# Kernel optimization log

Hardware: AMD Instinct MI355X
Metric: run time of the kernel (lower is better)

Reference implementation:

```python
import jax, jax.numpy as jnp
import numpy as np

K = 16          # max_points
S = 3           # num_scales
DM = 256        # d_model
KD = 16         # k_dim geometric projection
TAU = 1e-4
LN_EPS = 1e-5


def _boundaries():
    edges = [(i, j) for i in range(K) for j in range(i + 1, K)]
    tris = [(i, j, k) for i in range(K) for j in range(i + 1, K) for k in range(j + 1, K)]
    E, T = len(edges), len(tris)
    B1 = np.zeros((K, E), np.float32)
    for e, (i, j) in enumerate(edges):
        B1[i, e] = -1.0
        B1[j, e] = 1.0
    eidx = {e: n for n, e in enumerate(edges)}
    B2 = np.zeros((E, T), np.float32)
    for t, (i, j, k) in enumerate(tris):
        B2[eidx[(j, k)], t] = 1.0
        B2[eidx[(i, k)], t] = -1.0
        B2[eidx[(i, j)], t] = 1.0
    ei = np.array([e[0] for e in edges])
    ej = np.array([e[1] for e in edges])
    tij = np.array([eidx[(a, b)] for a, b, c in tris])
    tjk = np.array([eidx[(b, c)] for a, b, c in tris])
    tik = np.array([eidx[(a, c)] for a, b, c in tris])
    return (jnp.asarray(B1), jnp.asarray(B2), jnp.asarray(np.abs(B1)),
            jnp.asarray(ei), jnp.asarray(ej), jnp.asarray(tij), jnp.asarray(tjk), jnp.asarray(tik))

_B1, _B2, _ABS, _EI, _EJ, _TIJ, _TJK, _TIK = _boundaries()
E = _B1.shape[1]  # 120


def _ln(x, g, b):
    m = jnp.mean(x, -1, keepdims=True)
    v = jnp.mean((x - m) ** 2, -1, keepdims=True)
    return (x - m) * jax.lax.rsqrt(v + LN_EPS) * g + b


def setup_inputs() -> dict:
    key = jax.random.key(0)
    ks = jax.random.split(key, 12)
    B = 1024
    p = lambda k, *sh: 0.02 * jax.random.normal(k, sh, dtype=jnp.float32)
    return {
        'x': jax.random.normal(ks[0], (B, K, DM), dtype=jnp.float32),
        'mask': jnp.ones((B, K), dtype=jnp.float32),
        'Wg': p(ks[1], DM, KD), 'bg': jnp.zeros((KD,), jnp.float32),
        'log_scales': jnp.linspace(-1.5, 1.5, S, dtype=jnp.float32),
        'Wv': p(ks[2], DM, DM * S), 'bv': jnp.zeros((DM * S,), jnp.float32),
        'We': p(ks[3], DM, DM * S), 'be': jnp.zeros((DM * S,), jnp.float32),
        'Wo': p(ks[4], DM * S * 2, DM), 'bo': jnp.zeros((DM,), jnp.float32),
        'ln1_g': jnp.ones((DM,), jnp.float32), 'ln1_b': jnp.zeros((DM,), jnp.float32),
        'ln2_g': jnp.ones((DM,), jnp.float32), 'ln2_b': jnp.zeros((DM,), jnp.float32),
        'Wf1': p(ks[5], DM, DM * 4), 'bf1': jnp.zeros((DM * 4,), jnp.float32),
        'Wf2': p(ks[6], DM * 4, DM), 'bf2': jnp.zeros((DM,), jnp.float32),
    }


def reference(x, mask, Wg, bg, log_scales, Wv, bv, We, be, Wo, bo,
              ln1_g, ln1_b, ln2_g, ln2_b, Wf1, bf1, Wf2, bf2):
    B = x.shape[0]
    xn = _ln(x, ln1_g, ln1_b)
    P = xn @ Wg + bg                                   # [B,K,KD]
    m2 = mask[:, :, None] * mask[:, None, :]           # [B,K,K]
    p2 = jnp.sum(P * P, -1)
    Dsq = jnp.maximum(p2[:, :, None] + p2[:, None, :] - 2.0 * jnp.einsum('bkc,blc->bkl', P, P), 0.0) * m2
    sig2 = jnp.exp(log_scales) ** 2                    # [S]
    V0 = (xn @ Wv + bv).reshape(B, K, S, DM).transpose(0, 2, 1, 3)   # [B,S,K,D]
    Eraw = jnp.einsum('ke,bkd->bed', _ABS, xn)         # [B,E,D]
    Ein = (Eraw @ We + be).reshape(B, E, S, DM).transpose(0, 2, 1, 3)  # [B,S,E,D]
    aff = jnp.exp(-Dsq[:, None] / (2.0 * sig2[None, :, None, None] + 1e-8)) * m2[:, None]  # [B,S,K,K]
    W1 = aff[:, :, _EI, _EJ]                           # [B,S,E]
    W2 = W1[:, :, _TIJ] * W1[:, :, _TJK] * W1[:, :, _TIK]  # [B,S,T]
    L0 = jnp.einsum('ke,bse,le->bskl', _B1, W1, _B1) + TAU * jnp.eye(K, dtype=x.dtype)
    node_upd = jnp.einsum('bskl,bsld->bskd', L0, V0)
    term_down = jnp.einsum('ke,bk,kf->bef', _B1, mask, _B1)
    term_up = jnp.einsum('et,bst,ft->bsef', _B2, W2, _B2)
    L1 = term_down[:, None] + term_up + TAU * jnp.eye(E, dtype=x.dtype)
    edge_msg = jnp.einsum('bsef,bsfd->bsed', L1, Ein)
    edge_upd = jnp.einsum('ke,bsed->bskd', _ABS, edge_msg)
    nu = node_upd.transpose(0, 2, 1, 3).reshape(B, K, S * DM)
    eu = edge_upd.transpose(0, 2, 1, 3).reshape(B, K, S * DM)
    x = x + (jnp.concatenate([nu, eu], -1) @ Wo + bo)  # residual + attn_out (dropout=eval noop)
    h = _ln(x, ln2_g, ln2_b)
    return x + (jax.nn.gelu(h @ Wf1 + bf1, approximate=False) @ Wf2 + bf2)
```

## Files before the change

kernel.cpp:

```cpp
#include <hip/hip_runtime.h>
#include <hip/hip_bf16.h>
#include <cstdint>
#include <cstddef>

#define TAU 1e-4f
#define LN_EPS 1e-5f

typedef unsigned short ushort_t;
typedef unsigned int uint_t;
typedef __attribute__((ext_vector_type(8))) short short8;
typedef __attribute__((ext_vector_type(4))) float f32x4;

__device__ __forceinline__ ushort_t f2bf(float f) {
    union { float f; unsigned int u; } c; c.f = f;
    unsigned int r = (c.u + 0x7fffu + ((c.u >> 16) & 1u)) >> 16;
    return (ushort_t)r;
}
__device__ __forceinline__ void glds16(const void* g, void* l) {
    __builtin_amdgcn_global_load_lds((const __attribute__((address_space(1))) unsigned int*)g,
                                     (__attribute__((address_space(3))) unsigned int*)l,
                                     16, 0, 0);
}

__global__ __launch_bounds__(256) void kA(
    const float* __restrict__ xg, const float* __restrict__ maskg,
    const float* __restrict__ Wg, const float* __restrict__ bg,
    const float* __restrict__ ls, const float* __restrict__ g1,
    const float* __restrict__ b1, ushort_t* __restrict__ Mcat,
    float* __restrict__ gbuf,
    const float* __restrict__ Wv, const float* __restrict__ We,
    const float* __restrict__ Wo, const float* __restrict__ bv,
    const float* __restrict__ be, const float* __restrict__ Wf1,
    const float* __restrict__ Wf2, ushort_t* __restrict__ WcatT,
    ushort_t* __restrict__ Wf1T, ushort_t* __restrict__ Wf2T,
    float* __restrict__ cvpart, float* __restrict__ beWo) {
    __shared__ __align__(16) float POOL[7968];
    const int tid = threadIdx.x;

    if (blockIdx.x >= 1024) {
        const int id = blockIdx.x - 1024;
        if (id < 384) {
            float (*rowS)[256] = (float(*)[256])POOL;
            const int q0 = (id & 63) * 4;
            const int w = id >> 6;
            const int half = w / 3, s = w - half * 3;
            const float* src = half ? We : Wv;
#pragma unroll
            for (int r = 0; r < 4; ++r)
                rowS[r][tid] = src[(size_t)(q0 + r) * 768 + s * 256 + tid];
            __syncthreads();
            const float* wo = Wo + (size_t)(half * 768 + s * 256) * 256 + tid;
            float a0 = 0.f, a1 = 0.f, a2 = 0.f, a3 = 0.f;
            for (int d = 0; d < 256; ++d) {
                float wv = wo[(size_t)d * 256];
                a0 += rowS[0][d] * wv; a1 += rowS[1][d] * wv;
                a2 += rowS[2][d] * wv; a3 += rowS[3][d] * wv;
            }
            const int rt = half * 3 + s;
            ushort4 pk;
            pk.x = f2bf(a0); pk.y = f2bf(a1); pk.z = f2bf(a2); pk.w = f2bf(a3);
            *(ushort4*)&WcatT[(size_t)tid * 1536 + rt * 256 + q0] = pk;
        } else if (id < 390) {
            const int w = id - 384;
            const int half = w / 3, s = w - half * 3;
            const float* vec = half ? be : bv;
            POOL[tid] = vec[s * 256 + tid];
            __syncthreads();
            const float* wo = Wo + (size_t)(half * 768 + s * 256) * 256 + tid;
            float acc = 0.f;
            for (int d = 0; d < 256; ++d) acc += POOL[d] * wo[(size_t)d * 256];
            if (half) beWo[s * 256 + tid] = acc;
            else cvpart[s * 256 + tid] = acc;
        } else {
            float (*tS)[65] = (float(*)[65])POOL;
            const float* src; ushort_t* dst;
            int sr0, sc0, ss, dr0, dc0, ds_;
            if (id < 454) {
                int t = id - 390; int ki = t & 3, ni = t >> 2;
                src = Wf1; ss = 1024; sr0 = ki * 64; sc0 = ni * 64;
                dst = Wf1T; ds_ = 256; dr0 = ni * 64; dc0 = ki * 64;
            } else {
                int t = id - 454; int ki = t >> 2, ni = t & 3;
                src = Wf2; ss = 256; sr0 = ki * 64; sc0 = ni * 64;
                dst = Wf2T; ds_ = 1024; dr0 = ni * 64; dc0 = ki * 64;
            }
            const int rl = tid >> 6, cl = tid & 63;
#pragma unroll
            for (int p = 0; p < 16; ++p) {
                int r = p * 4 + rl;
                tS[r][cl] = src[(size_t)(sr0 + r) * ss + sc0 + cl];
            }
            __syncthreads();
#pragma unroll
            for (int p = 0; p < 16; ++p) {
                int r = p * 4 + rl;
                dst[(size_t)(dr0 + r) * ds_ + dc0 + cl] = f2bf(tS[cl][r]);
            }
        }
        return;
    }

    const int b = blockIdx.x;
    float (*XS)[260] = (float(*)[260])POOL;
    float (*WgTh)[132] = (float(*)[132])(POOL + 4160);
    float* Ms = POOL + 4160;
    float (*Wh)[16][17] = (float(*)[16][17])(POOL + 6272);
    float* Ts = POOL + 7088;
    float (*Pl)[17] = (float(*)[17])(POOL + 7136);
    float (*dotm)[17] = (float(*)[17])(POOL + 7408);
    float (*DsqS)[17] = (float(*)[17])(POOL + 7680);
    float* mk = POOL + 7952;

    const float* xb = xg + (size_t)b * 4096;
#pragma unroll
    for (int i = 0; i < 4; ++i) {
        int idx = tid * 4 + i * 1024;
        int k = idx >> 8, c = idx & 255;
        float4 v = *(const float4*)&xb[idx];
        XS[k][c] = v.x; XS[k][c + 1] = v.y; XS[k][c + 2] = v.z; XS[k][c + 3] = v.w;
    }
    if (tid < 16) mk[tid] = maskg[b * 16 + tid];
    __syncthreads();

    {
        const int k = tid >> 4, c = tid & 15;
        float s = 0.f;
#pragma unroll
        for (int j = 0; j < 16; ++j) s += XS[k][c + 16 * j];
        for (int off = 8; off; off >>= 1) s += __shfl_down(s, off, 16);
        float mean = __shfl(s, 0, 16) * (1.f / 256.f);
        float vs = 0.f;
#pragma unroll
        for (int j = 0; j < 16; ++j) { float d = XS[k][c + 16 * j] - mean; vs += d * d; }
        for (int off = 8; off; off >>= 1) vs += __shfl_down(vs, off, 16);
        float rstd = rsqrtf(__shfl(vs, 0, 16) * (1.f / 256.f) + LN_EPS);
#pragma unroll
        for (int j = 0; j < 16; ++j) {
            int cc = c + 16 * j;
            XS[k][cc] = (XS[k][cc] - mean) * rstd * g1[cc] + b1[cc];
        }
    }
    __syncthreads();

    {
        const int k = tid >> 4, c = tid & 15;
        const int ql = tid >> 1, hf = tid & 1;
        float acc = bg[c];
        {
            const float4* wp = (const float4*)(Wg + ql * 16 + hf * 8);
            float4 w0 = wp[0], w1 = wp[1];
            WgTh[hf * 8 + 0][ql] = w0.x; WgTh[hf * 8 + 1][ql] = w0.y;
            WgTh[hf * 8 + 2][ql] = w0.z; WgTh[hf * 8 + 3][ql] = w0.w;
            WgTh[hf * 8 + 4][ql] = w1.x; WgTh[hf * 8 + 5][ql] = w1.y;
            WgTh[hf * 8 + 6][ql] = w1.z; WgTh[hf * 8 + 7][ql] = w1.w;
        }
        __syncthreads();
        const float4* wp2 = (const float4*)(Wg + (128 + ql) * 16 + hf * 8);
        float4 w20 = wp2[0], w21 = wp2[1];
#pragma unroll
        for (int q4 = 0; q4 < 32; ++q4) {
            float4 wv = *(const float4*)&WgTh[c][q4 * 4];
            float4 xv = *(const float4*)&XS[k][q4 * 4];
            acc += wv.x * xv.x + wv.y * xv.y + wv.z * xv.z + wv.w * xv.w;
        }
        __syncthreads();
        WgTh[hf * 8 + 0][ql] = w20.x; WgTh[hf * 8 + 1][ql] = w20.y;
        WgTh[hf * 8 + 2][ql] = w20.z; WgTh[hf * 8 + 3][ql] = w20.w;
        WgTh[hf * 8 + 4][ql] = w21.x; WgTh[hf * 8 + 5][ql] = w21.y;
        WgTh[hf * 8 + 6][ql] = w21.z; WgTh[hf * 8 + 7][ql] = w21.w;
        __syncthreads();
#pragma unroll
        for (int q4 = 0; q4 < 32; ++q4) {
            float4 wv = *(const float4*)&WgTh[c][q4 * 4];
            float4 xv = *(const float4*)&XS[k][128 + q4 * 4];
            acc += wv.x * xv.x + wv.y * xv.y + wv.z * xv.z + wv.w * xv.w;
        }
        Pl[k][c] = acc;
    }
    __syncthreads();
    const int k = tid >> 4, m = tid & 15;
    {
        float d = 0.f;
#pragma unroll
        for (int c = 0; c < 16; ++c) d += Pl[k][c] * Pl[m][c];
        dotm[k][m] = d;
    }
    __syncthreads();
    {
        float v = dotm[k][k] + dotm[m][m] - 2.f * dotm[k][m];
        DsqS[k][m] = fmaxf(v, 0.f) * mk[k] * mk[m];
    }
    {
        float d = DsqS[k][m];
        float mm = mk[k] * mk[m];
#pragma unroll
        for (int s = 0; s < 3; ++s) {
            float i2 = 1.f / (2.f * expf(2.f * ls[s]) + 1e-8f);
            Wh[s][k][m] = (k == m) ? 0.f : expf(-d * i2) * mm;
        }
    }
    __syncthreads();
    if (tid < 48) {
        int s = tid >> 4, j = tid & 15;
        float t = 0.f;
        for (int i = 0; i < j; ++i) {
            float d = 0.f;
            for (int jj = j + 1; jj < 16; ++jj) d += Wh[s][j][jj] * Wh[s][i][jj];
            t += Wh[s][i][j] * d;
        }
        Ts[s * 16 + j] = t;
    }
    __syncthreads();
    float gd = 0.f;
#pragma unroll
    for (int o = 0; o < 16; ++o) {
        if (o == m) continue;
        int u = o < m ? o : m, v = o < m ? m : o;
        float gu = (u == k) ? (float)(2 * k - 15) : ((u > k) ? 1.f : -1.f);
        float gv = (v == k) ? (float)(2 * k - 15) : ((v > k) ? 1.f : -1.f);
        gd += -gu * mk[u] + gv * mk[v];
        if (u == k || v == k) gd += TAU;
    }
#pragma unroll
    for (int s = 0; s < 3; ++s) {
        float rs = 0.f;
#pragma unroll
        for (int o = 0; o < 16; ++o) rs += Wh[s][k][o];
        float l0 = (k == m) ? (rs + TAU) : -Wh[s][k][m];
        float G = gd + ((k == m) ? 4.f * Ts[s * 16 + k] : 0.f);
        Ms[s * 256 + tid] = l0;
        Ms[768 + s * 256 + tid] = G;
        float gg = G;
        for (int off = 8; off; off >>= 1) gg += __shfl_down(gg, off, 16);
        if (m == 0) gbuf[b * 48 + k * 3 + s] = 0.5f * gg;
    }
    __syncthreads();

    {
        const int q2 = (tid & 127) * 2;
        const int rtbase = (tid >> 7) * 3;
        float xv0[16], xv1[16];
#pragma unroll
        for (int l = 0; l < 16; ++l) { xv0[l] = XS[l][q2]; xv1[l] = XS[l][q2 + 1]; }
        const size_t obase = (size_t)b * 16 * 1536;
#pragma unroll
        for (int rtt = 0; rtt < 3; ++rtt) {
            const int rt = rtbase + rtt;
#pragma unroll
            for (int kk = 0; kk < 16; ++kk) {
                const float4* mp = (const float4*)&Ms[rt * 256 + kk * 16];
                float4 m0 = mp[0], m1 = mp[1], m2 = mp[2], m3 = mp[3];
                float a0 = m0.x * xv0[0] + m0.y * xv0[1] + m0.z * xv0[2] + m0.w * xv0[3]
                         + m1.x * xv0[4] + m1.y * xv0[5] + m1.z * xv0[6] + m1.w * xv0[7]
                         + m2.x * xv0[8] + m2.y * xv0[9] + m2.z * xv0[10] + m2.w * xv0[11]
                         + m3.x * xv0[12] + m3.y * xv0[13] + m3.z * xv0[14] + m3.w * xv0[15];
                float a1 = m0.x * xv1[0] + m0.y * xv1[1] + m0.z * xv1[2] + m0.w * xv1[3]
                         + m1.x * xv1[4] + m1.y * xv1[5] + m1.z * xv1[6] + m1.w * xv1[7]
                         + m2.x * xv1[8] + m2.y * xv1[9] + m2.z * xv1[10] + m2.w * xv1[11]
                         + m3.x * xv1[12] + m3.y * xv1[13] + m3.z * xv1[14] + m3.w * xv1[15];
                uint_t pk = (uint_t)f2bf(a0) | ((uint_t)f2bf(a1) << 16);
                *(uint_t*)&Mcat[obase + (size_t)kk * 1536 + rt * 256 + q2] = pk;
            }
        }
    }
}

__device__ __forceinline__ void gemm64_db(
    const ushort_t* __restrict__ A, const ushort_t* __restrict__ Bt,
    int Kdim, int m0, int n0, f32x4 acc[2][4],
    ushort_t (*As0)[32], ushort_t (*As1)[32],
    ushort_t (*Bs0)[32], ushort_t (*Bs1)[32]) {
    const int tid = threadIdx.x;
    const int wave = tid >> 6, lane = tid & 63;
    const int lq = lane >> 4, lr = lane & 15;
    const int wm = wave >> 1, wn = wave & 1;
    const int r = tid >> 2, ca = (tid & 3) << 3;
    const ushort_t* Ag  = A  + (size_t)(m0 + r) * Kdim + ca;
    const ushort_t* Bg0 = Bt + (size_t)(n0 + r) * Kdim + ca;
    const ushort_t* Bg1 = Bt + (size_t)(n0 + 64 + r) * Kdim + ca;
    char* aD0  = (char*)As0 + wave * 1024;
    char* aD1  = (char*)As1 + wave * 1024;
    char* b0D0 = (char*)Bs0 + wave * 1024;
    char* b0D1 = (char*)Bs0 + 4096 + wave * 1024;
    char* b1D0 = (char*)Bs1 + wave * 1024;
    char* b1D1 = (char*)Bs1 + 4096 + wave * 1024;

    glds16(Ag, aD0); glds16(Bg0, b0D0); glds16(Bg1, b0D1);

    for (int kt = 0; kt < Kdim; kt += 64) {
        {
            const int kn = kt + 32;
            if (kn < Kdim) {
                glds16(Ag + kn, aD1); glds16(Bg0 + kn, b1D0); glds16(Bg1 + kn, b1D1);
                asm volatile("s_waitcnt vmcnt(3)" ::: "memory");
            } else {
                asm volatile("s_waitcnt vmcnt(0)" ::: "memory");
            }
            __builtin_amdgcn_s_barrier();
            short8 af[2], bfr[4];
#pragma unroll
            for (int i = 0; i < 2; ++i) af[i] = *(const short8*)&As0[wm * 32 + i * 16 + lr][lq * 8];
#pragma unroll
            for (int j = 0; j < 4; ++j) bfr[j] = *(const short8*)&Bs0[wn * 64 + j * 16 + lr][lq * 8];
#pragma unroll
            for (int i = 0; i < 2; ++i)
#pragma unroll
                for (int j = 0; j < 4; ++j)
                    acc[i][j] = __builtin_amdgcn_mfma_f32_16x16x32_bf16(af[i], bfr[j], acc[i][j], 0, 0, 0);
            asm volatile("s_waitcnt lgkmcnt(0)" ::: "memory");
            __builtin_amdgcn_s_barrier();
        }
        {
            const int kn = kt + 64;
            if (kn < Kdim) {
                glds16(Ag + kn, aD0); glds16(Bg0 + kn, b0D0); glds16(Bg1 + kn, b0D1);
                asm volatile("s_waitcnt vmcnt(3)" ::: "memory");
            } else {
                asm volatile("s_waitcnt vmcnt(0)" ::: "memory");
            }
            __builtin_amdgcn_s_barrier();
            short8 af[2], bfr[4];
#pragma unroll
            for (int i = 0; i < 2; ++i) af[i] = *(const short8*)&As1[wm * 32 + i * 16 + lr][lq * 8];
#pragma unroll
            for (int j = 0; j < 4; ++j) bfr[j] = *(const short8*)&Bs1[wn * 64 + j * 16 + lr][lq * 8];
#pragma unroll
            for (int i = 0; i < 2; ++i)
#pragma unroll
                for (int j = 0; j < 4; ++j)
                    acc[i][j] = __builtin_amdgcn_mfma_f32_16x16x32_bf16(af[i], bfr[j], acc[i][j], 0, 0, 0);
            asm volatile("s_waitcnt lgkmcnt(0)" ::: "memory");
            __builtin_amdgcn_s_barrier();
        }
    }
}

__global__ __launch_bounds__(256) void kZY_gemm(
    const ushort_t* __restrict__ Mcat, const ushort_t* __restrict__ WcatT,
    const float* __restrict__ xin, const float* __restrict__ bo,
    const float* __restrict__ cvpart, const float* __restrict__ beWo,
    const float* __restrict__ gbuf, float* __restrict__ xp) {
    __shared__ ushort_t As0[64][32], As1[64][32];
    __shared__ ushort_t Bs0[128][32], Bs1[128][32];
    __shared__ float cvS[128], bewS[3][128], gblk[64][3];
    const int tid = threadIdx.x;
    const int m0 = blockIdx.x * 64, n0 = blockIdx.y * 128;
    if (tid < 128) {
        int n = n0 + tid;
        cvS[tid] = bo[n] + TAU * (cvpart[n] + cvpart[256 + n] + cvpart[512 + n]);
        bewS[0][tid] = beWo[n];
        bewS[1][tid] = beWo[256 + n];
        bewS[2][tid] = beWo[512 + n];
    }
    if (tid < 192) { int rr = tid / 3, s = tid - rr * 3; gblk[rr][s] = gbuf[(size_t)(m0 + rr) * 3 + s]; }
    f32x4 acc[2][4] = {};
    gemm64_db(Mcat, WcatT, 1536, m0, n0, acc, As0, As1, Bs0, Bs1);
    const int wave = tid >> 6, lane = tid & 63, lq = lane >> 4, lr = lane & 15;
    const int wm = wave >> 1, wn = wave & 1;
#pragma unroll
    for (int i = 0; i < 2; ++i)
#pragma unroll
        for (int j = 0; j < 4; ++j) {
            int nl = wn * 64 + j * 16 + lr;
#pragma unroll
            for (int v = 0; v < 4; ++v) {
                int rl = wm * 32 + i * 16 + lq * 4 + v;
                size_t idx = (size_t)(m0 + rl) * 256 + n0 + nl;
                xp[idx] = acc[i][j][v] + xin[idx] + cvS[nl] +
                          gblk[rl][0] * bewS[0][nl] + gblk[rl][1] * bewS[1][nl] +
                          gblk[rl][2] * bewS[2][nl];
            }
        }
}

__global__ __launch_bounds__(256) void k_ln2(const float* __restrict__ xp,
                                             const float* __restrict__ g2,
                                             const float* __restrict__ b2,
                                             ushort_t* __restrict__ h) {
    const int tid = threadIdx.x;
    const int row = blockIdx.x * 4 + (tid >> 6);
    const int lane = tid & 63;
    const float* xr = xp + (size_t)row * 256;
    float v0 = xr[lane], v1 = xr[lane + 64], v2 = xr[lane + 128], v3 = xr[lane + 192];
    float s = v0 + v1 + v2 + v3;
    for (int m = 32; m; m >>= 1) s += __shfl_xor(s, m, 64);
    float mean = s * (1.f / 256.f);
    float d0 = v0 - mean, d1 = v1 - mean, d2 = v2 - mean, d3 = v3 - mean;
    float q = d0 * d0 + d1 * d1 + d2 * d2 + d3 * d3;
    for (int m = 32; m; m >>= 1) q += __shfl_xor(q, m, 64);
    float rstd = rsqrtf(q * (1.f / 256.f) + LN_EPS);
    ushort_t* hr = h + (size_t)row * 256;
    hr[lane] = f2bf(d0 * rstd * g2[lane] + b2[lane]);
    hr[lane + 64] = f2bf(d1 * rstd * g2[lane + 64] + b2[lane + 64]);
    hr[lane + 128] = f2bf(d2 * rstd * g2[lane + 128] + b2[lane + 128]);
    hr[lane + 192] = f2bf(d3 * rstd * g2[lane + 192] + b2[lane + 192]);
}

__global__ __launch_bounds__(256) void k3_gemm(const ushort_t* __restrict__ h,
                                               const ushort_t* __restrict__ Wf1T,
                                               const float* __restrict__ bf1,
                                               ushort_t* __restrict__ F1g) {
    __shared__ ushort_t As0[64][32], As1[64][32];
    __shared__ ushort_t Bs0[128][32], Bs1[128][32];
    const int tid = threadIdx.x;
    const int m0 = blockIdx.x * 64, n0 = blockIdx.y * 128;
    f32x4 acc[2][4] = {};
    gemm64_db(h, Wf1T, 256, m0, n0, acc, As0, As1, Bs0, Bs1);
    const int wave = tid >> 6, lane = tid & 63, lq = lane >> 4, lr = lane & 15;
    const int wm = wave >> 1, wn = wave & 1;
#pragma unroll
    for (int i = 0; i < 2; ++i)
#pragma unroll
        for (int j = 0; j < 4; ++j) {
            int n = n0 + wn * 64 + j * 16 + lr;
            float bn = bf1[n];
#pragma unroll
            for (int v = 0; v < 4; ++v) {
                int rg = m0 + wm * 32 + i * 16 + lq * 4 + v;
                float u = acc[i][j][v] + bn;
                float gl = 0.5f * u * (1.f + erff(u * 0.70710678118f));
                F1g[(size_t)rg * 1024 + n] = f2bf(gl);
            }
        }
}

__global__ __launch_bounds__(256) void k4_gemm(const ushort_t* __restrict__ F1g,
                                               const ushort_t* __restrict__ Wf2T,
                                               const float* __restrict__ bf2,
                                               const float* __restrict__ xp,
                                               float* __restrict__ out) {
    __shared__ ushort_t As0[64][32], As1[64][32];
    __shared__ ushort_t Bs0[128][32], Bs1[128][32];
    const int tid = threadIdx.x;
    const int m0 = blockIdx.x * 64, n0 = blockIdx.y * 128;
    f32x4 acc[2][4] = {};
    gemm64_db(F1g, Wf2T, 1024, m0, n0, acc, As0, As1, Bs0, Bs1);
    const int wave = tid >> 6, lane = tid & 63, lq = lane >> 4, lr = lane & 15;
    const int wm = wave >> 1, wn = wave & 1;
#pragma unroll
    for (int i = 0; i < 2; ++i)
#pragma unroll
        for (int j = 0; j < 4; ++j) {
            int n = n0 + wn * 64 + j * 16 + lr;
            float bn = bf2[n];
#pragma unroll
            for (int v = 0; v < 4; ++v) {
                size_t idx = (size_t)(m0 + wm * 32 + i * 16 + lq * 4 + v) * 256 + n;
                out[idx] = xp[idx] + acc[i][j][v] + bn;
            }
        }
}

extern "C" void kernel_launch(void* const* d_in, const int* in_sizes, int n_in,
                              void* d_out, int out_size, void* d_ws, size_t ws_size,
                              hipStream_t stream) {
    const float* x = (const float*)d_in[0];
    const float* mask = (const float*)d_in[1];
    const float* Wg = (const float*)d_in[2];
    const float* bg = (const float*)d_in[3];
    const float* ls = (const float*)d_in[4];
    const float* Wv = (const float*)d_in[5];
    const float* bv = (const float*)d_in[6];
    const float* We = (const float*)d_in[7];
    const float* be = (const float*)d_in[8];
    const float* Wo = (const float*)d_in[9];
    const float* bo = (const float*)d_in[10];
    const float* g1 = (const float*)d_in[11];
    const float* b1 = (const float*)d_in[12];
    const float* g2 = (const float*)d_in[13];
    const float* b2 = (const float*)d_in[14];
    const float* Wf1 = (const float*)d_in[15];
    const float* bf1 = (const float*)d_in[16];
    const float* Wf2 = (const float*)d_in[17];
    const float* bf2 = (const float*)d_in[18];
    float* out = (float*)d_out;

    char* ws = (char*)d_ws;
    ushort_t* Mcat = (ushort_t*)(ws);
    ushort_t* F1g = (ushort_t*)(ws);
    ushort_t* WcatT = (ushort_t*)(ws + 50331648);
    ushort_t* Wf1T = (ushort_t*)(ws + 51118080);
    ushort_t* Wf2T = (ushort_t*)(ws + 51642368);
    float* cvpart = (float*)(ws + 52166656);
    float* beWo = (float*)(ws + 52169728);
    float* gbuf = (float*)(ws + 52172800);
    float* xp = (float*)(ws + 52369408);
    ushort_t* h = (ushort_t*)(ws + 69146624);

    kA<<<dim3(1542), dim3(256), 0, stream>>>(x, mask, Wg, bg, ls, g1, b1,
                                             Mcat, gbuf,
                                             Wv, We, Wo, bv, be, Wf1, Wf2,
                                             WcatT, Wf1T, Wf2T, cvpart, beWo);
    kZY_gemm<<<dim3(256, 2), dim3(256), 0, stream>>>(Mcat, WcatT, x, bo, cvpart, beWo, gbuf, xp);
    k_ln2<<<dim3(4096), dim3(256), 0, stream>>>(xp, g2, b2, h);
    k3_gemm<<<dim3(256, 8), dim3(256), 0, stream>>>(h, Wf1T, bf1, F1g);
    k4_gemm<<<dim3(256, 2), dim3(256), 0, stream>>>(F1g, Wf2T, bf2, xp, out);
}
```

Measured before the change: 207.2 us.

## Split-K the Mcat GEMM into two partials and fuse reduction into LN2

The 16384x256x1536 GEMM launches 512 blocks, which is only about two blocks per CU. It is now split along K into two halves written to fp32 partial buffers, doubling the block count to 1024. The bias, residual and g-weighted beWo epilogue moves into the LayerNorm kernel, which sums the two partials, writes xp and normalizes. This adds two 16 MB fp32 partial writes and reads to raise occupancy on the long-K GEMM.

```diff
diff --git a/kernel.cpp b/kernel.cpp
--- a/kernel.cpp
+++ b/kernel.cpp
@@ -265,9 +265,9 @@
     }
 }
 
-__device__ __forceinline__ void gemm64_db(
+__device__ __forceinline__ void gemm64_dbs(
     const ushort_t* __restrict__ A, const ushort_t* __restrict__ Bt,
-    int Kdim, int m0, int n0, f32x4 acc[2][4],
+    int Kstride, int Klen, int m0, int n0, f32x4 acc[2][4],
     ushort_t (*As0)[32], ushort_t (*As1)[32],
     ushort_t (*Bs0)[32], ushort_t (*Bs1)[32]) {
     const int tid = threadIdx.x;
@@ -275,9 +275,9 @@
     const int lq = lane >> 4, lr = lane & 15;
     const int wm = wave >> 1, wn = wave & 1;
     const int r = tid >> 2, ca = (tid & 3) << 3;
-    const ushort_t* Ag  = A  + (size_t)(m0 + r) * Kdim + ca;
-    const ushort_t* Bg0 = Bt + (size_t)(n0 + r) * Kdim + ca;
-    const ushort_t* Bg1 = Bt + (size_t)(n0 + 64 + r) * Kdim + ca;
+    const ushort_t* Ag  = A  + (size_t)(m0 + r) * Kstride + ca;
+    const ushort_t* Bg0 = Bt + (size_t)(n0 + r) * Kstride + ca;
+    const ushort_t* Bg1 = Bt + (size_t)(n0 + 64 + r) * Kstride + ca;
     char* aD0  = (char*)As0 + wave * 1024;
     char* aD1  = (char*)As1 + wave * 1024;
     char* b0D0 = (char*)Bs0 + wave * 1024;
@@ -287,10 +287,10 @@
 
     glds16(Ag, aD0); glds16(Bg0, b0D0); glds16(Bg1, b0D1);
 
-    for (int kt = 0; kt < Kdim; kt += 64) {
+    for (int kt = 0; kt < Klen; kt += 64) {
         {
             const int kn = kt + 32;
-            if (kn < Kdim) {
+            if (kn < Klen) {
                 glds16(Ag + kn, aD1); glds16(Bg0 + kn, b1D0); glds16(Bg1 + kn, b1D1);
                 asm volatile("s_waitcnt vmcnt(3)" ::: "memory");
             } else {
@@ -312,7 +312,7 @@
         }
         {
             const int kn = kt + 64;
-            if (kn < Kdim) {
+            if (kn < Klen) {
                 glds16(Ag + kn, aD0); glds16(Bg0 + kn, b0D0); glds16(Bg1 + kn, b0D1);
                 asm volatile("s_waitcnt vmcnt(3)" ::: "memory");
             } else {
@@ -335,61 +335,62 @@
     }
 }
 
-__global__ __launch_bounds__(256) void kZY_gemm(
+__global__ __launch_bounds__(256) void kZY_part(
     const ushort_t* __restrict__ Mcat, const ushort_t* __restrict__ WcatT,
+    float* __restrict__ P0, float* __restrict__ P1) {
+    __shared__ ushort_t As0[64][32], As1[64][32];
+    __shared__ ushort_t Bs0[128][32], Bs1[128][32];
+    const int tid = threadIdx.x;
+    const int m0 = blockIdx.x * 64, n0 = blockIdx.y * 128;
+    const int koff = blockIdx.z * 768;
+    f32x4 acc[2][4] = {};
+    gemm64_dbs(Mcat + koff, WcatT + koff, 1536, 768, m0, n0, acc, As0, As1, Bs0, Bs1);
+    float* P = blockIdx.z ? P1 : P0;
+    const int wave = tid >> 6, lane = tid & 63, lq = lane >> 4, lr = lane & 15;
+    const int wm = wave >> 1, wn = wave & 1;
+#pragma unroll
+    for (int i = 0; i < 2; ++i)
+#pragma unroll
+        for (int j = 0; j < 4; ++j) {
+            int nl = wn * 64 + j * 16 + lr;
+#pragma unroll
+            for (int v = 0; v < 4; ++v) {
+                int rl = wm * 32 + i * 16 + lq * 4 + v;
+                P[(size_t)(m0 + rl) * 256 + n0 + nl] = acc[i][j][v];
+            }
+        }
+}
+
+__global__ __launch_bounds__(256) void k_ln2c(
+    const float* __restrict__ P0, const float* __restrict__ P1,
     const float* __restrict__ xin, const float* __restrict__ bo,
     const float* __restrict__ cvpart, const float* __restrict__ beWo,
-    const float* __restrict__ gbuf, float* __restrict__ xp) {
-    __shared__ ushort_t As0[64][32], As1[64][32];
-    __shared__ ushort_t Bs0[128][32], Bs1[128][32];
-    __shared__ float cvS[128], bewS[3][128], gblk[64][3];
-    const int tid = threadIdx.x;
-    const int m0 = blockIdx.x * 64, n0 = blockIdx.y * 128;
-    if (tid < 128) {
-        int n = n0 + tid;
-        cvS[tid] = bo[n] + TAU * (cvpart[n] + cvpart[256 + n] + cvpart[512 + n]);
-        bewS[0][tid] = beWo[n];
-        bewS[1][tid] = beWo[256 + n];
-        bewS[2][tid] = beWo[512 + n];
-    }
-    if (tid < 192) { int rr = tid / 3, s = tid - rr * 3; gblk[rr][s] = gbuf[(size_t)(m0 + rr) * 3 + s]; }
-    f32x4 acc[2][4] = {};
-    gemm64_db(Mcat, WcatT, 1536, m0, n0, acc, As0, As1, Bs0, Bs1);
-    const int wave = tid >> 6, lane = tid & 63, lq = lane >> 4, lr = lane & 15;
-    const int wm = wave >> 1, wn = wave & 1;
-#pragma unroll
-    for (int i = 0; i < 2; ++i)
-#pragma unroll
-        for (int j = 0; j < 4; ++j) {
-            int nl = wn * 64 + j * 16 + lr;
-#pragma unroll
-            for (int v = 0; v < 4; ++v) {
-                int rl = wm * 32 + i * 16 + lq * 4 + v;
-                size_t idx = (size_t)(m0 + rl) * 256 + n0 + nl;
-                xp[idx] = acc[i][j][v] + xin[idx] + cvS[nl] +
-                          gblk[rl][0] * bewS[0][nl] + gblk[rl][1] * bewS[1][nl] +
-                          gblk[rl][2] * bewS[2][nl];
-            }
-        }
-}
-
-__global__ __launch_bounds__(256) void k_ln2(const float* __restrict__ xp,
-                                             const float* __restrict__ g2,
-                                             const float* __restrict__ b2,
-                                             ushort_t* __restrict__ h) {
+    const float* __restrict__ gbuf, const float* __restrict__ g2,
+    const float* __restrict__ b2, float* __restrict__ xp,
+    ushort_t* __restrict__ h) {
     const int tid = threadIdx.x;
     const int row = blockIdx.x * 4 + (tid >> 6);
     const int lane = tid & 63;
-    const float* xr = xp + (size_t)row * 256;
-    float v0 = xr[lane], v1 = xr[lane + 64], v2 = xr[lane + 128], v3 = xr[lane + 192];
-    float s = v0 + v1 + v2 + v3;
+    const float* gp = gbuf + (size_t)row * 3;
+    const float ga = gp[0], gb = gp[1], gc = gp[2];
+    const size_t base = (size_t)row * 256;
+    float v[4];
+#pragma unroll
+    for (int c4 = 0; c4 < 4; ++c4) {
+        const int col = lane + c4 * 64;
+        float cv = bo[col] + TAU * (cvpart[col] + cvpart[256 + col] + cvpart[512 + col]);
+        v[c4] = P0[base + col] + P1[base + col] + xin[base + col] + cv
+              + ga * beWo[col] + gb * beWo[256 + col] + gc * beWo[512 + col];
+        xp[base + col] = v[c4];
+    }
+    float s = v[0] + v[1] + v[2] + v[3];
     for (int m = 32; m; m >>= 1) s += __shfl_xor(s, m, 64);
     float mean = s * (1.f / 256.f);
-    float d0 = v0 - mean, d1 = v1 - mean, d2 = v2 - mean, d3 = v3 - mean;
+    float d0 = v[0] - mean, d1 = v[1] - mean, d2 = v[2] - mean, d3 = v[3] - mean;
     float q = d0 * d0 + d1 * d1 + d2 * d2 + d3 * d3;
     for (int m = 32; m; m >>= 1) q += __shfl_xor(q, m, 64);
     float rstd = rsqrtf(q * (1.f / 256.f) + LN_EPS);
-    ushort_t* hr = h + (size_t)row * 256;
+    ushort_t* hr = h + base;
     hr[lane] = f2bf(d0 * rstd * g2[lane] + b2[lane]);
     hr[lane + 64] = f2bf(d1 * rstd * g2[lane + 64] + b2[lane + 64]);
     hr[lane + 128] = f2bf(d2 * rstd * g2[lane + 128] + b2[lane + 128]);
@@ -405,7 +406,7 @@
     const int tid = threadIdx.x;
     const int m0 = blockIdx.x * 64, n0 = blockIdx.y * 128;
     f32x4 acc[2][4] = {};
-    gemm64_db(h, Wf1T, 256, m0, n0, acc, As0, As1, Bs0, Bs1);
+    gemm64_dbs(h, Wf1T, 256, 256, m0, n0, acc, As0, As1, Bs0, Bs1);
     const int wave = tid >> 6, lane = tid & 63, lq = lane >> 4, lr = lane & 15;
     const int wm = wave >> 1, wn = wave & 1;
 #pragma unroll
@@ -434,7 +435,7 @@
     const int tid = threadIdx.x;
     const int m0 = blockIdx.x * 64, n0 = blockIdx.y * 128;
     f32x4 acc[2][4] = {};
-    gemm64_db(F1g, Wf2T, 1024, m0, n0, acc, As0, As1, Bs0, Bs1);
+    gemm64_dbs(F1g, Wf2T, 1024, 1024, m0, n0, acc, As0, As1, Bs0, Bs1);
     const int wave = tid >> 6, lane = tid & 63, lq = lane >> 4, lr = lane & 15;
     const int wm = wave >> 1, wn = wave & 1;
 #pragma unroll
@@ -486,13 +487,16 @@
     float* gbuf = (float*)(ws + 52172800);
     float* xp = (float*)(ws + 52369408);
     ushort_t* h = (ushort_t*)(ws + 69146624);
+    float* P0 = (float*)(ws + 77535232);
+    float* P1 = (float*)(ws + 94312448);
 
     kA<<<dim3(1542), dim3(256), 0, stream>>>(x, mask, Wg, bg, ls, g1, b1,
                                              Mcat, gbuf,
                                              Wv, We, Wo, bv, be, Wf1, Wf2,
                                              WcatT, Wf1T, Wf2T, cvpart, beWo);
-    kZY_gemm<<<dim3(256, 2), dim3(256), 0, stream>>>(Mcat, WcatT, x, bo, cvpart, beWo, gbuf, xp);
-    k_ln2<<<dim3(4096), dim3(256), 0, stream>>>(xp, g2, b2, h);
+    kZY_part<<<dim3(256, 2, 2), dim3(256), 0, stream>>>(Mcat, WcatT, P0, P1);
+    k_ln2c<<<dim3(4096), dim3(256), 0, stream>>>(P0, P1, x, bo, cvpart, beWo,
+                                                 gbuf, g2, b2, xp, h);
     k3_gemm<<<dim3(256, 8), dim3(256), 0, stream>>>(h, Wf1T, bf1, F1g);
     k4_gemm<<<dim3(256, 2), dim3(256), 0, stream>>>(F1g, Wf2T, bf2, xp, out);
 }
```

Result: slower. 212.1 us (+2.4%).
